# Kernel tuning notes

Hardware: AMD Instinct MI355X
Metric: run time of the kernel (lower is better)

Reference implementation:

```python
import jax, jax.numpy as jnp
import numpy as np

D = 1024      # input_dim / hidden_size
H = 16        # n_heads
HD = D // H   # head_size = 64
F = 4096      # mlp_dim
EPS = 1e-6


def setup_inputs() -> dict:
    key = jax.random.key(0)
    ks = jax.random.split(key, 16)
    s = 0.02
    inp = {
        "x": jax.random.normal(ks[0], (4, 2048, D), dtype=jnp.float32),
        # attention params (torch Linear: y = x @ W.T + b; we store W as [out,in])
        "Wq": jax.random.normal(ks[1], (D, D), dtype=jnp.float32) * s,
        "bq": jax.random.normal(ks[2], (D,), dtype=jnp.float32) * s,
        "Wk": jax.random.normal(ks[3], (D, D), dtype=jnp.float32) * s,
        "bk": jax.random.normal(ks[4], (D,), dtype=jnp.float32) * s,
        "Wv": jax.random.normal(ks[5], (D, D), dtype=jnp.float32) * s,
        "bv": jax.random.normal(ks[6], (D,), dtype=jnp.float32) * s,
        "Wo": jax.random.normal(ks[7], (D, D), dtype=jnp.float32) * s,
        "bo": jax.random.normal(ks[8], (D,), dtype=jnp.float32) * s,
        # MLP params
        "W1": jax.random.normal(ks[9], (F, D), dtype=jnp.float32) * s,
        "b1": jax.random.normal(ks[10], (F,), dtype=jnp.float32) * s,
        "W2": jax.random.normal(ks[11], (D, F), dtype=jnp.float32) * s,
        "b2": jax.random.normal(ks[12], (D,), dtype=jnp.float32) * s,
        # LayerNorm params
        "ln1_g": jnp.ones((D,), dtype=jnp.float32),
        "ln1_b": jnp.zeros((D,), dtype=jnp.float32),
        "ln2_g": jnp.ones((D,), dtype=jnp.float32),
        "ln2_b": jnp.zeros((D,), dtype=jnp.float32),
    }
    return inp


def _layernorm(x, g, b):
    mu = jnp.mean(x, axis=-1, keepdims=True)
    var = jnp.mean(jnp.square(x - mu), axis=-1, keepdims=True)
    return (x - mu) * jax.lax.rsqrt(var + EPS) * g + b


def reference(x, Wq, bq, Wk, bk, Wv, bv, Wo, bo, W1, b1, W2, b2,
              ln1_g, ln1_b, ln2_g, ln2_b):
    B, S, _ = x.shape
    h = x
    xn = _layernorm(x, ln1_g, ln1_b)
    # Q/K/V projections -> [B, H, S, HD]
    def split_heads(t):
        return t.reshape(B, S, H, HD).transpose(0, 2, 1, 3)
    q = split_heads(xn @ Wq.T + bq)
    k = split_heads(xn @ Wk.T + bk)
    v = split_heads(xn @ Wv.T + bv)
    scores = jnp.einsum('bhqd,bhkd->bhqk', q, k) / np.sqrt(HD).astype(np.float32)
    probs = jax.nn.softmax(scores, axis=-1)
    ctx = jnp.einsum('bhqk,bhkd->bhqd', probs, v)      # [B,H,S,HD]
    ctx = ctx.transpose(0, 2, 1, 3).reshape(B, S, D)
    attn_out = ctx @ Wo.T + bo
    x = attn_out + h
    h = x
    xn = _layernorm(x, ln2_g, ln2_b)
    y = jax.nn.gelu(xn @ W1.T + b1, approximate=False)  # torch nn.GELU() = exact erf gelu
    y = y @ W2.T + b2
    return y + h
```

## Files before the change

kernel.cpp:

```cpp
#include <hip/hip_runtime.h>
#include <hip/hip_bf16.h>
#include <math.h>

typedef __attribute__((ext_vector_type(8))) short short8;
typedef __attribute__((ext_vector_type(4))) float f32x4;

#define MFMA_BF16 __builtin_amdgcn_mfma_f32_16x16x32_bf16

__device__ __forceinline__ ushort f2bf(float f) {
  union { __hip_bfloat16 h; ushort u; } c;
  c.h = __float2bfloat16(f);
  return c.u;
}
__device__ __forceinline__ void async_cp16(const ushort* g, ushort* l) {
  __builtin_amdgcn_global_load_lds(
      (const __attribute__((address_space(1))) void*)g,
      (__attribute__((address_space(3))) void*)l, 16, 0, 0);
}

__global__ __launch_bounds__(256) void conv_all(
    const float* __restrict__ Wq, const float* __restrict__ Wk,
    const float* __restrict__ Wv, const float* __restrict__ Wo,
    const float* __restrict__ W1, const float* __restrict__ W2,
    const float* __restrict__ bq, const float* __restrict__ bk,
    const float* __restrict__ bv,
    ushort* __restrict__ wqkv, ushort* __restrict__ wo,
    ushort* __restrict__ w1, ushort* __restrict__ w2,
    float* __restrict__ bqkv) {
  int i = blockIdx.x * 256 + threadIdx.x;
  if (i < 3145728) {
    const float* src; ushort* dst; int off;
    if (i < 786432)        {
      dst = wqkv; off = i;
      if (i < 262144)      src = Wq + (size_t)i * 4;
      else if (i < 524288) src = Wk + (size_t)(i - 262144) * 4;
      else                 src = Wv + (size_t)(i - 524288) * 4;
    } else if (i < 1048576) { dst = wo; off = i - 786432;  src = Wo + (size_t)off * 4; }
    else if (i < 2097152)   { dst = w1; off = i - 1048576; src = W1 + (size_t)off * 4; }
    else                    { dst = w2; off = i - 2097152; src = W2 + (size_t)off * 4; }
    float4 v = *(const float4*)src;
    ushort4 o;
    o.x = f2bf(v.x); o.y = f2bf(v.y); o.z = f2bf(v.z); o.w = f2bf(v.w);
    ((ushort4*)dst)[off] = o;
  } else if (i < 3146496) {
    int off = i - 3145728;
    const float* src;
    if (off < 256)      src = bq + (size_t)off * 4;
    else if (off < 512) src = bk + (size_t)(off - 256) * 4;
    else                src = bv + (size_t)(off - 512) * 4;
    ((float4*)bqkv)[off] = *(const float4*)src;
  }
}

__global__ __launch_bounds__(256) void ln_kernel(const float* __restrict__ x,
    const float* __restrict__ g, const float* __restrict__ b,
    ushort* __restrict__ out) {
  const int row = blockIdx.x, t = threadIdx.x;
  float4 v = ((const float4*)(x + (size_t)row * 1024))[t];
  float s  = v.x + v.y + v.z + v.w;
  float ss = v.x*v.x + v.y*v.y + v.z*v.z + v.w*v.w;
  #pragma unroll
  for (int off = 32; off >= 1; off >>= 1) {
    s  += __shfl_xor(s, off);
    ss += __shfl_xor(ss, off);
  }
  __shared__ float red[8];
  int wv = t >> 6, ln = t & 63;
  if (ln == 0) { red[wv] = s; red[4 + wv] = ss; }
  __syncthreads();
  float S  = red[0] + red[1] + red[2] + red[3];
  float SS = red[4] + red[5] + red[6] + red[7];
  float mu  = S * (1.0f/1024.0f);
  float var = SS * (1.0f/1024.0f) - mu*mu;
  float rs  = rsqrtf(var + 1e-6f);
  float4 gv = ((const float4*)g)[t];
  float4 bv = ((const float4*)b)[t];
  ushort4 o;
  o.x = f2bf((v.x-mu)*rs*gv.x + bv.x);
  o.y = f2bf((v.y-mu)*rs*gv.y + bv.y);
  o.z = f2bf((v.z-mu)*rs*gv.z + bv.z);
  o.w = f2bf((v.w-mu)*rs*gv.w + bv.w);
  ((ushort4*)(out + (size_t)row*1024))[t] = o;
}

enum { EPI_QK = 0, EPI_VT = 1, EPI_WO = 2, EPI_GELU = 3, EPI_OUT = 4 };

template <int EPI>
__global__ __launch_bounds__(512, 2) void gemm256_kernel(const ushort* __restrict__ A,
    const ushort* __restrict__ Bw, const float* __restrict__ bias,
    void* __restrict__ outp, void* __restrict__ outp2, int K, int N, float scale) {
  __shared__ ushort As[2][256 * 64];
  __shared__ ushort Bs[2][256 * 64];
  const int t = threadIdx.x;
  const int lane = t & 63, wave = t >> 6;
  const int col = lane & 15, quad = lane >> 4;
  const int m0 = blockIdx.x * 256, n0 = blockIdx.y * 256;
  const int wm = wave >> 2, wn = wave & 3;

  f32x4 acc[8][4];
  #pragma unroll
  for (int i = 0; i < 8; i++)
    #pragma unroll
    for (int j = 0; j < 4; j++)
      acc[i][j] = (f32x4){0.f, 0.f, 0.f, 0.f};

  size_t aoff[2], boff[2];
  int d0[2];
  #pragma unroll
  for (int i = 0; i < 2; i++) {
    int c = i * 512 + t, r = c >> 3, p = c & 7;
    aoff[i] = (size_t)(m0 + r) * K + (p ^ (r & 7)) * 8;
    boff[i] = (size_t)(n0 + r) * K + (p ^ (r & 7)) * 8;
    d0[i] = c * 8;
  }
  const size_t up = (size_t)128 * K;

  const int NT = K >> 6;
  #pragma unroll
  for (int i = 0; i < 2; i++) async_cp16(A  + aoff[i],      &As[0][d0[i]]);
  #pragma unroll
  for (int i = 0; i < 2; i++) async_cp16(Bw + boff[i],      &Bs[0][d0[i]]);
  #pragma unroll
  for (int i = 0; i < 2; i++) async_cp16(A  + aoff[i] + up, &As[0][8192 + d0[i]]);
  #pragma unroll
  for (int i = 0; i < 2; i++) async_cp16(Bw + boff[i] + up, &Bs[0][8192 + d0[i]]);
  asm volatile("s_waitcnt vmcnt(4)" ::: "memory");
  __builtin_amdgcn_sched_barrier(0);
  __builtin_amdgcn_s_barrier();
  __builtin_amdgcn_sched_barrier(0);

  short8 af0[4][2], af1[4][2], bf[2][2];
  for (int kt = 0; kt < NT; kt++) {
    const int cur = kt & 1, nxt = cur ^ 1;
    const size_t ko = (size_t)(kt + 1) << 6;
    const bool more = (kt + 1 < NT);

    #pragma unroll
    for (int tml = 0; tml < 4; tml++) {
      const int row = wm * 64 + tml * 16 + col;
      #pragma unroll
      for (int c = 0; c < 2; c++)
        af0[tml][c] = *(const short8*)&As[cur][row * 64 + (((c * 4 + quad) ^ (row & 7)) * 8)];
    }
    #pragma unroll
    for (int tnl = 0; tnl < 2; tnl++) {
      const int row = wn * 32 + tnl * 16 + col;
      #pragma unroll
      for (int c = 0; c < 2; c++)
        bf[tnl][c] = *(const short8*)&Bs[cur][row * 64 + (((c * 4 + quad) ^ (row & 7)) * 8)];
    }
    if (more) {
      #pragma unroll
      for (int i = 0; i < 2; i++) async_cp16(A + aoff[i] + ko, &As[nxt][d0[i]]);
      asm volatile("s_waitcnt vmcnt(4)" ::: "memory");
    } else {
      asm volatile("s_waitcnt vmcnt(2)" ::: "memory");
    }
    __builtin_amdgcn_sched_barrier(0);
    __builtin_amdgcn_s_barrier();
    asm volatile("s_waitcnt lgkmcnt(0)" ::: "memory");
    __builtin_amdgcn_sched_barrier(0);
    __builtin_amdgcn_s_setprio(1);
    #pragma unroll
    for (int tml = 0; tml < 4; tml++)
      #pragma unroll
      for (int tnl = 0; tnl < 2; tnl++) {
        acc[tml][tnl] = MFMA_BF16(af0[tml][0], bf[tnl][0], acc[tml][tnl], 0, 0, 0);
        acc[tml][tnl] = MFMA_BF16(af0[tml][1], bf[tnl][1], acc[tml][tnl], 0, 0, 0);
      }
    __builtin_amdgcn_s_setprio(0);
    __builtin_amdgcn_sched_barrier(0);
    __builtin_amdgcn_s_barrier();
    __builtin_amdgcn_sched_barrier(0);

    #pragma unroll
    for (int tml = 0; tml < 4; tml++) {
      const int row = 128 + wm * 64 + tml * 16 + col;
      #pragma unroll
      for (int c = 0; c < 2; c++)
        af1[tml][c] = *(const short8*)&As[cur][row * 64 + (((c * 4 + quad) ^ (row & 7)) * 8)];
    }
    if (more) {
      #pragma unroll
      for (int i = 0; i < 2; i++) async_cp16(Bw + boff[i] + ko, &Bs[nxt][d0[i]]);
      asm volatile("s_waitcnt vmcnt(4)" ::: "memory");
    } else {
      asm volatile("s_waitcnt vmcnt(0)" ::: "memory");
    }
    __builtin_amdgcn_sched_barrier(0);
    __builtin_amdgcn_s_barrier();
    asm volatile("s_waitcnt lgkmcnt(0)" ::: "memory");
    __builtin_amdgcn_sched_barrier(0);
    __builtin_amdgcn_s_setprio(1);
    #pragma unroll
    for (int tml = 0; tml < 4; tml++)
      #pragma unroll
      for (int tnl = 0; tnl < 2; tnl++) {
        acc[4+tml][tnl] = MFMA_BF16(af1[tml][0], bf[tnl][0], acc[4+tml][tnl], 0, 0, 0);
        acc[4+tml][tnl] = MFMA_BF16(af1[tml][1], bf[tnl][1], acc[4+tml][tnl], 0, 0, 0);
      }
    __builtin_amdgcn_s_setprio(0);
    __builtin_amdgcn_sched_barrier(0);
    __builtin_amdgcn_s_barrier();
    __builtin_amdgcn_sched_barrier(0);

    #pragma unroll
    for (int tnl = 0; tnl < 2; tnl++) {
      const int row = 128 + wn * 32 + tnl * 16 + col;
      #pragma unroll
      for (int c = 0; c < 2; c++)
        bf[tnl][c] = *(const short8*)&Bs[cur][row * 64 + (((c * 4 + quad) ^ (row & 7)) * 8)];
    }
    if (more) {
      #pragma unroll
      for (int i = 0; i < 2; i++) async_cp16(A + aoff[i] + up + ko, &As[nxt][8192 + d0[i]]);
      asm volatile("s_waitcnt vmcnt(4)" ::: "memory");
    } else {
      asm volatile("s_waitcnt vmcnt(0)" ::: "memory");
    }
    __builtin_amdgcn_sched_barrier(0);
    __builtin_amdgcn_s_barrier();
    asm volatile("s_waitcnt lgkmcnt(0)" ::: "memory");
    __builtin_amdgcn_sched_barrier(0);
    __builtin_amdgcn_s_setprio(1);
    #pragma unroll
    for (int tml = 0; tml < 4; tml++)
      #pragma unroll
      for (int tnl = 0; tnl < 2; tnl++) {
        acc[tml][2+tnl] = MFMA_BF16(af0[tml][0], bf[tnl][0], acc[tml][2+tnl], 0, 0, 0);
        acc[tml][2+tnl] = MFMA_BF16(af0[tml][1], bf[tnl][1], acc[tml][2+tnl], 0, 0, 0);
      }
    __builtin_amdgcn_s_setprio(0);
    __builtin_amdgcn_sched_barrier(0);
    __builtin_amdgcn_s_barrier();
    __builtin_amdgcn_sched_barrier(0);

    if (more) {
      #pragma unroll
      for (int i = 0; i < 2; i++) async_cp16(Bw + boff[i] + up + ko, &Bs[nxt][8192 + d0[i]]);
      asm volatile("s_waitcnt vmcnt(4)" ::: "memory");
    } else {
      asm volatile("s_waitcnt vmcnt(0)" ::: "memory");
    }
    __builtin_amdgcn_sched_barrier(0);
    __builtin_amdgcn_s_barrier();
    asm volatile("s_waitcnt lgkmcnt(0)" ::: "memory");
    __builtin_amdgcn_sched_barrier(0);
    __builtin_amdgcn_s_setprio(1);
    #pragma unroll
    for (int tml = 0; tml < 4; tml++)
      #pragma unroll
      for (int tnl = 0; tnl < 2; tnl++) {
        acc[4+tml][2+tnl] = MFMA_BF16(af1[tml][0], bf[tnl][0], acc[4+tml][2+tnl], 0, 0, 0);
        acc[4+tml][2+tnl] = MFMA_BF16(af1[tml][1], bf[tnl][1], acc[4+tml][2+tnl], 0, 0, 0);
      }
    __builtin_amdgcn_s_setprio(0);
    __builtin_amdgcn_sched_barrier(0);
    __builtin_amdgcn_s_barrier();
    __builtin_amdgcn_sched_barrier(0);
  }

  #pragma unroll
  for (int tm = 0; tm < 8; tm++) {
    const int ha = tm >> 2, tml = tm & 3;
    #pragma unroll
    for (int tn = 0; tn < 4; tn++) {
      const int hb = tn >> 1, tnl = tn & 1;
      const int n = n0 + hb * 128 + wn * 32 + tnl * 16 + col;
      const float bn = bias[n];
      #pragma unroll
      for (int r = 0; r < 4; r++) {
        const int m = m0 + ha * 128 + wm * 64 + tml * 16 + quad * 4 + r;
        float v = acc[tm][tn][r] + bn;
        if (EPI == EPI_QK) {
          int nl = n & 1023, h = nl >> 6, hd = nl & 63;
          int bb = m >> 11, s2 = m & 2047;
          if (n < 1024)
            ((ushort*)outp)[(((size_t)(bb * 16 + h) * 2048 + s2) * 64) + hd] = f2bf(v * scale);
          else
            ((ushort*)outp2)[(((size_t)(bb * 16 + h) * 2048 + s2) * 64) + hd] = f2bf(v);
        } else {
          float u = v * 0.7978845608028654f * (1.0f + 0.044715f * v * v);
          float e = __builtin_amdgcn_exp2f(u * 2.885390081777927f);
          float th = 1.0f - 2.0f * __builtin_amdgcn_rcpf(e + 1.0f);
          ((ushort*)outp)[(size_t)m * N + n] = f2bf(0.5f * v * (1.0f + th));
        }
      }
    }
  }
}

template <int EPI>
__global__ __launch_bounds__(512, 2) void gemmW_kernel(const ushort* __restrict__ A,
    const ushort* __restrict__ Bw, const float* __restrict__ bias,
    const float* __restrict__ res, void* __restrict__ outp, int K, int N) {
  __shared__ ushort As[2][256 * 64];
  __shared__ ushort Bs[2][128 * 64];
  const int t = threadIdx.x;
  const int lane = t & 63, wave = t >> 6;
  const int col = lane & 15, quad = lane >> 4;
  const int m0 = blockIdx.x * 256, n0 = blockIdx.y * 128;
  const int wm = wave >> 1, wn = wave & 1;

  f32x4 acc[4][4];
  #pragma unroll
  for (int i = 0; i < 4; i++)
    #pragma unroll
    for (int j = 0; j < 4; j++)
      acc[i][j] = (f32x4){0.f, 0.f, 0.f, 0.f};

  size_t aoff[2];
  int ad0[2];
  #pragma unroll
  for (int i = 0; i < 2; i++) {
    int c = i * 512 + t, r = c >> 3, p = c & 7;
    aoff[i] = (size_t)(m0 + r) * K + (p ^ (r & 7)) * 8;
    ad0[i] = c * 8;
  }
  size_t boff;
  int bd0;
  {
    int c = t, r = c >> 3, p = c & 7;
    boff = (size_t)(n0 + r) * K + (p ^ (r & 7)) * 8;
    bd0 = c * 8;
  }
  const size_t upA = (size_t)128 * K;
  const size_t upB = (size_t)64 * K;

  const int NT = K >> 6;
  #pragma unroll
  for (int i = 0; i < 2; i++) async_cp16(A + aoff[i], &As[0][ad0[i]]);
  async_cp16(Bw + boff, &Bs[0][bd0]);
  #pragma unroll
  for (int i = 0; i < 2; i++) async_cp16(A + aoff[i] + upA, &As[0][8192 + ad0[i]]);
  async_cp16(Bw + boff + upB, &Bs[0][4096 + bd0]);
  asm volatile("s_waitcnt vmcnt(3)" ::: "memory");
  __builtin_amdgcn_sched_barrier(0);
  __builtin_amdgcn_s_barrier();
  __builtin_amdgcn_sched_barrier(0);

  short8 af0[2][2], af1[2][2], bf[2][2];
  for (int kt = 0; kt < NT; kt++) {
    const int cur = kt & 1, nxt = cur ^ 1;
    const size_t ko = (size_t)(kt + 1) << 6;
    const bool more = (kt + 1 < NT);

    #pragma unroll
    for (int tml = 0; tml < 2; tml++) {
      const int row = wm * 32 + tml * 16 + col;
      #pragma unroll
      for (int c = 0; c < 2; c++)
        af0[tml][c] = *(const short8*)&As[cur][row * 64 + (((c * 4 + quad) ^ (row & 7)) * 8)];
    }
    #pragma unroll
    for (int tnl = 0; tnl < 2; tnl++) {
      const int row = wn * 32 + tnl * 16 + col;
      #pragma unroll
      for (int c = 0; c < 2; c++)
        bf[tnl][c] = *(const short8*)&Bs[cur][row * 64 + (((c * 4 + quad) ^ (row & 7)) * 8)];
    }
    if (more) {
      #pragma unroll
      for (int i = 0; i < 2; i++) async_cp16(A + aoff[i] + ko, &As[nxt][ad0[i]]);
      asm volatile("s_waitcnt vmcnt(3)" ::: "memory");
    } else {
      asm volatile("s_waitcnt vmcnt(1)" ::: "memory");
    }
    __builtin_amdgcn_sched_barrier(0);
    __builtin_amdgcn_s_barrier();
    asm volatile("s_waitcnt lgkmcnt(0)" ::: "memory");
    __builtin_amdgcn_sched_barrier(0);
    __builtin_amdgcn_s_setprio(1);
    #pragma unroll
    for (int tml = 0; tml < 2; tml++)
      #pragma unroll
      for (int tnl = 0; tnl < 2; tnl++) {
        acc[tml][tnl] = MFMA_BF16(af0[tml][0], bf[tnl][0], acc[tml][tnl], 0, 0, 0);
        acc[tml][tnl] = MFMA_BF16(af0[tml][1], bf[tnl][1], acc[tml][tnl], 0, 0, 0);
      }
    __builtin_amdgcn_s_setprio(0);
    __builtin_amdgcn_sched_barrier(0);
    __builtin_amdgcn_s_barrier();
    __builtin_amdgcn_sched_barrier(0);

    #pragma unroll
    for (int tml = 0; tml < 2; tml++) {
      const int row = 128 + wm * 32 + tml * 16 + col;
      #pragma unroll
      for (int c = 0; c < 2; c++)
        af1[tml][c] = *(const short8*)&As[cur][row * 64 + (((c * 4 + quad) ^ (row & 7)) * 8)];
    }
    if (more) {
      async_cp16(Bw + boff + ko, &Bs[nxt][bd0]);
      asm volatile("s_waitcnt vmcnt(3)" ::: "memory");
    } else {
      asm volatile("s_waitcnt vmcnt(0)" ::: "memory");
    }
    __builtin_amdgcn_sched_barrier(0);
    __builtin_amdgcn_s_barrier();
    asm volatile("s_waitcnt lgkmcnt(0)" ::: "memory");
    __builtin_amdgcn_sched_barrier(0);
    __builtin_amdgcn_s_setprio(1);
    #pragma unroll
    for (int tml = 0; tml < 2; tml++)
      #pragma unroll
      for (int tnl = 0; tnl < 2; tnl++) {
        acc[2+tml][tnl] = MFMA_BF16(af1[tml][0], bf[tnl][0], acc[2+tml][tnl], 0, 0, 0);
        acc[2+tml][tnl] = MFMA_BF16(af1[tml][1], bf[tnl][1], acc[2+tml][tnl], 0, 0, 0);
      }
    __builtin_amdgcn_s_setprio(0);
    __builtin_amdgcn_sched_barrier(0);
    __builtin_amdgcn_s_barrier();
    __builtin_amdgcn_sched_barrier(0);

    #pragma unroll
    for (int tnl = 0; tnl < 2; tnl++) {
      const int row = 64 + wn * 32 + tnl * 16 + col;
      #pragma unroll
      for (int c = 0; c < 2; c++)
        bf[tnl][c] = *(const short8*)&Bs[cur][4096 + ((row - 64) * 64) + (((c * 4 + quad) ^ (row & 7)) * 8)];
    }
    if (more) {
      #pragma unroll
      for (int i = 0; i < 2; i++) async_cp16(A + aoff[i] + upA + ko, &As[nxt][8192 + ad0[i]]);
      asm volatile("s_waitcnt vmcnt(5)" ::: "memory");
    } else {
      asm volatile("s_waitcnt vmcnt(0)" ::: "memory");
    }
    __builtin_amdgcn_sched_barrier(0);
    __builtin_amdgcn_s_barrier();
    asm volatile("s_waitcnt lgkmcnt(0)" ::: "memory");
    __builtin_amdgcn_sched_barrier(0);
    __builtin_amdgcn_s_setprio(1);
    #pragma unroll
    for (int tml = 0; tml < 2; tml++)
      #pragma unroll
      for (int tnl = 0; tnl < 2; tnl++) {
        acc[tml][2+tnl] = MFMA_BF16(af0[tml][0], bf[tnl][0], acc[tml][2+tnl], 0, 0, 0);
        acc[tml][2+tnl] = MFMA_BF16(af0[tml][1], bf[tnl][1], acc[tml][2+tnl], 0, 0, 0);
      }
    __builtin_amdgcn_s_setprio(0);
    __builtin_amdgcn_sched_barrier(0);
    __builtin_amdgcn_s_barrier();
    __builtin_amdgcn_sched_barrier(0);

    if (more) {
      async_cp16(Bw + boff + upB + ko, &Bs[nxt][4096 + bd0]);
      asm volatile("s_waitcnt vmcnt(3)" ::: "memory");
    } else {
      asm volatile("s_waitcnt vmcnt(0)" ::: "memory");
    }
    __builtin_amdgcn_sched_barrier(0);
    __builtin_amdgcn_s_barrier();
    asm volatile("s_waitcnt lgkmcnt(0)" ::: "memory");
    __builtin_amdgcn_sched_barrier(0);
    __builtin_amdgcn_s_setprio(1);
    #pragma unroll
    for (int tml = 0; tml < 2; tml++)
      #pragma unroll
      for (int tnl = 0; tnl < 2; tnl++) {
        acc[2+tml][2+tnl] = MFMA_BF16(af1[tml][0], bf[tnl][0], acc[2+tml][2+tnl], 0, 0, 0);
        acc[2+tml][2+tnl] = MFMA_BF16(af1[tml][1], bf[tnl][1], acc[2+tml][2+tnl], 0, 0, 0);
      }
    __builtin_amdgcn_s_setprio(0);
    __builtin_amdgcn_sched_barrier(0);
    __builtin_amdgcn_s_barrier();
    __builtin_amdgcn_sched_barrier(0);
  }

  #pragma unroll
  for (int tm = 0; tm < 4; tm++) {
    const int ha = tm >> 1, tml = tm & 1;
    #pragma unroll
    for (int tn = 0; tn < 4; tn++) {
      const int hb = tn >> 1, tnl = tn & 1;
      const int n = n0 + hb * 64 + wn * 32 + tnl * 16 + col;
      #pragma unroll
      for (int r = 0; r < 4; r++) {
        const int m = m0 + ha * 128 + wm * 32 + tml * 16 + quad * 4 + r;
        float v = acc[tm][tn][r];
        if (EPI == EPI_VT) {
          float vv = v + bias[m];
          int h = m >> 6, hd = m & 63, bb = n >> 11, s2 = n & 2047;
          ((ushort*)outp)[((size_t)((bb * 16 + h) * 64 + hd)) * 2048 + s2] = f2bf(vv);
        } else {
          ((float*)outp)[(size_t)m * N + n] = v + bias[n] + res[(size_t)m * N + n];
        }
      }
    }
  }
}

__global__ __launch_bounds__(256) void attn_kernel(const ushort* __restrict__ Qb,
    const ushort* __restrict__ Kb, const ushort* __restrict__ Vt,
    ushort* __restrict__ ctx) {
  const int lane = threadIdx.x & 63, wave = threadIdx.x >> 6;
  const int col = lane & 15, quad = lane >> 4;
  const int bx = blockIdx.x;
  const int bh = bx & 63;
  const int qt = bx >> 6;
  const int qbase = qt * 128 + wave * 32;
  const ushort* Qh = Qb + (size_t)bh * 2048 * 64;
  const ushort* Kh = Kb + (size_t)bh * 2048 * 64;
  const ushort* Vh = Vt + (size_t)bh * 64 * 2048;

  short8 qa[2][2];
  #pragma unroll
  for (int qg = 0; qg < 2; qg++) {
    const ushort* Qr = Qh + (size_t)(qbase + qg * 16 + col) * 64 + quad * 8;
    qa[qg][0] = *(const short8*)Qr;
    qa[qg][1] = *(const short8*)(Qr + 32);
  }

  short8 ones8;
  #pragma unroll
  for (int i = 0; i < 8; i++) ones8[i] = (short)0x3F80;

  f32x4 Ot[2][4], Ol[2];
  #pragma unroll
  for (int qg = 0; qg < 2; qg++) {
    Ol[qg] = (f32x4){0.f, 0.f, 0.f, 0.f};
    #pragma unroll
    for (int dt = 0; dt < 4; dt++) Ot[qg][dt] = (f32x4){0.f, 0.f, 0.f, 0.f};
  }

  __shared__ ushort Ks[2][2][64 * 32];
  __shared__ ushort Vs[2][2][64 * 32];
  __shared__ ushort P_lds[4][16][64];

  const int lrow = lane >> 2;
  const int srow = wave * 16 + lrow;
  const int lcol = ((lane & 3) ^ ((srow >> 1) & 3)) * 8;
  const ushort* Kg = Kh + (size_t)srow * 64 + lcol;
  const ushort* Vg = Vh + (size_t)srow * 2048 + lcol;
  const int so = (wave * 16) * 32;

  const int kvswz = (col >> 1) & 3;
  const int pswz = col & 7;

  async_cp16(Kg,      &Ks[0][0][so]);
  async_cp16(Kg + 32, &Ks[0][1][so]);
  async_cp16(Vg,      &Vs[0][0][so]);
  async_cp16(Vg + 32, &Vs[0][1][so]);
  __syncthreads();

  int cur = 0;
  for (int kb = 0; kb < 2048; kb += 64) {
    if (kb + 64 < 2048) {
      const int nxt = cur ^ 1;
      async_cp16(Kg + (size_t)(kb + 64) * 64,      &Ks[nxt][0][so]);
      async_cp16(Kg + (size_t)(kb + 64) * 64 + 32, &Ks[nxt][1][so]);
      async_cp16(Vg + (kb + 64),                   &Vs[nxt][0][so]);
      async_cp16(Vg + (kb + 64) + 32,              &Vs[nxt][1][so]);
    }

    short8 kf[4][2], vf[4][2];
    #pragma unroll
    for (int kt = 0; kt < 4; kt++)
      #pragma unroll
      for (int c = 0; c < 2; c++)
        kf[kt][c] = *(const short8*)&Ks[cur][c][(kt * 16 + col) * 32 + (quad ^ kvswz) * 8];
    #pragma unroll
    for (int dt = 0; dt < 4; dt++)
      #pragma unroll
      for (int c = 0; c < 2; c++)
        vf[dt][c] = *(const short8*)&Vs[cur][c][(dt * 16 + col) * 32 + (quad ^ kvswz) * 8];

    #pragma unroll
    for (int qg = 0; qg < 2; qg++) {
      f32x4 s[4];
      __builtin_amdgcn_s_setprio(1);
      #pragma unroll
      for (int kt = 0; kt < 4; kt++) {
        s[kt] = (f32x4){0.f, 0.f, 0.f, 0.f};
        s[kt] = MFMA_BF16(kf[kt][0], qa[qg][0], s[kt], 0, 0, 0);
        s[kt] = MFMA_BF16(kf[kt][1], qa[qg][1], s[kt], 0, 0, 0);
      }
      __builtin_amdgcn_s_setprio(0);
      ushort(*P)[64] = P_lds[wave];
      #pragma unroll
      for (int kt = 0; kt < 4; kt++) {
        float p0 = __builtin_amdgcn_exp2f(s[kt][0]);
        float p1 = __builtin_amdgcn_exp2f(s[kt][1]);
        float p2 = __builtin_amdgcn_exp2f(s[kt][2]);
        float p3 = __builtin_amdgcn_exp2f(s[kt][3]);
        uint2 pk;
        asm("v_cvt_pk_bf16_f32 %0, %1, %2" : "=v"(pk.x) : "v"(p0), "v"(p1));
        asm("v_cvt_pk_bf16_f32 %0, %1, %2" : "=v"(pk.y) : "v"(p2), "v"(p3));
        *(uint2*)&P[col][(((2 * kt + (quad >> 1)) ^ pswz) * 8) + (quad & 1) * 4] = pk;
      }
      #pragma unroll
      for (int c = 0; c < 2; c++) {
        short8 pf = *(const short8*)&P_lds[wave][col][((4 * c + quad) ^ pswz) * 8];
        __builtin_amdgcn_s_setprio(1);
        #pragma unroll
        for (int dt = 0; dt < 4; dt++)
          Ot[qg][dt] = MFMA_BF16(vf[dt][c], pf, Ot[qg][dt], 0, 0, 0);
        Ol[qg] = MFMA_BF16(ones8, pf, Ol[qg], 0, 0, 0);
        __builtin_amdgcn_s_setprio(0);
      }
    }
    __syncthreads();
    cur ^= 1;
  }

  const int bb = bh >> 4, h = bh & 15;
  #pragma unroll
  for (int qg = 0; qg < 2; qg++) {
    float inv = __builtin_amdgcn_rcpf(Ol[qg][0]);
    const int q = qbase + qg * 16 + col;
    size_t base = ((size_t)(bb * 2048 + q)) * 1024 + h * 64;
    #pragma unroll
    for (int dt = 0; dt < 4; dt++) {
      ushort4 o;
      o.x = f2bf(Ot[qg][dt][0] * inv);
      o.y = f2bf(Ot[qg][dt][1] * inv);
      o.z = f2bf(Ot[qg][dt][2] * inv);
      o.w = f2bf(Ot[qg][dt][3] * inv);
      *(ushort4*)&ctx[base + dt * 16 + quad * 4] = o;
    }
  }
}

extern "C" void kernel_launch(void* const* d_in, const int* in_sizes, int n_in,
                              void* d_out, int out_size, void* d_ws, size_t ws_size,
                              hipStream_t stream) {
  const float* x     = (const float*)d_in[0];
  const float* Wq    = (const float*)d_in[1];
  const float* bq    = (const float*)d_in[2];
  const float* Wk    = (const float*)d_in[3];
  const float* bk    = (const float*)d_in[4];
  const float* Wv    = (const float*)d_in[5];
  const float* bv    = (const float*)d_in[6];
  const float* Wo    = (const float*)d_in[7];
  const float* bo    = (const float*)d_in[8];
  const float* W1    = (const float*)d_in[9];
  const float* b1    = (const float*)d_in[10];
  const float* W2    = (const float*)d_in[11];
  const float* b2    = (const float*)d_in[12];
  const float* ln1_g = (const float*)d_in[13];
  const float* ln1_b = (const float*)d_in[14];
  const float* ln2_g = (const float*)d_in[15];
  const float* ln2_b = (const float*)d_in[16];

  const size_t MB = 1ull << 20;
  char* ws = (char*)d_ws;
  ushort* Wqkv_b = (ushort*)(ws + 0 * MB);
  ushort* Wo_b   = (ushort*)(ws + 6 * MB);
  ushort* W1_b   = (ushort*)(ws + 8 * MB);
  ushort* W2_b   = (ushort*)(ws + 16 * MB);
  ushort* xn1    = (ushort*)(ws + 24 * MB);
  ushort* Qb     = (ushort*)(ws + 40 * MB);
  ushort* Kb     = (ushort*)(ws + 56 * MB);
  ushort* Vt     = (ushort*)(ws + 72 * MB);
  ushort* ctxb   = (ushort*)(ws + 88 * MB);
  float*  x2     = (float*)(ws + 104 * MB);
  ushort* xn2    = (ushort*)(ws + 136 * MB);
  ushort* y1     = (ushort*)(ws + 152 * MB);
  float*  bqkv   = (float*)(ws + 152 * MB);

  conv_all<<<12291, 256, 0, stream>>>(Wq, Wk, Wv, Wo, W1, W2, bq, bk, bv,
                                      Wqkv_b, Wo_b, W1_b, W2_b, bqkv);

  ln_kernel<<<8192, 256, 0, stream>>>(x, ln1_g, ln1_b, xn1);

  const float cs = 0.125f * 1.4426950408889634f;
  gemm256_kernel<EPI_QK><<<dim3(32, 8), 512, 0, stream>>>(
      xn1, Wqkv_b, bqkv, Qb, Kb, 1024, 2048, cs);
  gemmW_kernel<EPI_VT><<<dim3(4, 64), 512, 0, stream>>>(
      Wqkv_b + (size_t)2048 * 1024, xn1, bqkv + 2048, nullptr, Vt, 1024, 8192);

  attn_kernel<<<1024, 256, 0, stream>>>(Qb, Kb, Vt, ctxb);

  gemmW_kernel<EPI_WO><<<dim3(32, 8), 512, 0, stream>>>(
      ctxb, Wo_b, bo, x, x2, 1024, 1024);

  ln_kernel<<<8192, 256, 0, stream>>>(x2, ln2_g, ln2_b, xn2);

  gemm256_kernel<EPI_GELU><<<dim3(32, 16), 512, 0, stream>>>(
      xn2, W1_b, b1, y1, nullptr, 1024, 4096, 1.0f);
  gemmW_kernel<EPI_OUT><<<dim3(32, 8), 512, 0, stream>>>(
      y1, W2_b, b2, x2, d_out, 4096, 1024);
}
```

Measured before the change: 518.6 us.

## Transpose GEMM tile to 128x256 with 2x4 waves and XCD-aware block remap

Replaces the 256x128 gemmW kernel with a gemmH kernel that uses a 128(M)x256(N) tile, a 2x4 wave layout where each wave holds 64x64, and two MFMA phases per k-step instead of four. It also swizzles the 1D block index so that consecutive blocks on the same XCD share tiles, aiming at better L2 reuse. The goal is fewer barriers per k-step and more register reuse of A fragments, at the cost of a changed load/wait schedule and a remapped grid that must divide evenly for each launch.

```diff
diff --git a/kernel.cpp b/kernel.cpp
--- a/kernel.cpp
+++ b/kernel.cpp
@@ -291,16 +291,17 @@
 }
 
 template <int EPI>
-__global__ __launch_bounds__(512, 2) void gemmW_kernel(const ushort* __restrict__ A,
+__global__ __launch_bounds__(512, 2) void gemmH_kernel(const ushort* __restrict__ A,
     const ushort* __restrict__ Bw, const float* __restrict__ bias,
-    const float* __restrict__ res, void* __restrict__ outp, int K, int N) {
-  __shared__ ushort As[2][256 * 64];
-  __shared__ ushort Bs[2][128 * 64];
+    const float* __restrict__ res, void* __restrict__ outp, int K, int N, int gx) {
+  __shared__ ushort As[2][128 * 64];
+  __shared__ ushort Bs[2][256 * 64];
   const int t = threadIdx.x;
   const int lane = t & 63, wave = t >> 6;
   const int col = lane & 15, quad = lane >> 4;
-  const int m0 = blockIdx.x * 256, n0 = blockIdx.y * 128;
-  const int wm = wave >> 1, wn = wave & 1;
+  const int bl = (blockIdx.x & 7) * 32 + (blockIdx.x >> 3);
+  const int m0 = (bl % gx) * 128, n0 = (bl / gx) * 256;
+  const int wm = wave >> 2, wn = wave & 3;
 
   f32x4 acc[4][4];
   #pragma unroll
@@ -309,48 +310,41 @@
     for (int j = 0; j < 4; j++)
       acc[i][j] = (f32x4){0.f, 0.f, 0.f, 0.f};
 
-  size_t aoff[2];
-  int ad0[2];
+  size_t aoff[2], boff[2];
+  int ad0[2], bd0[2];
   #pragma unroll
   for (int i = 0; i < 2; i++) {
     int c = i * 512 + t, r = c >> 3, p = c & 7;
     aoff[i] = (size_t)(m0 + r) * K + (p ^ (r & 7)) * 8;
-    ad0[i] = c * 8;
-  }
-  size_t boff;
-  int bd0;
-  {
-    int c = t, r = c >> 3, p = c & 7;
-    boff = (size_t)(n0 + r) * K + (p ^ (r & 7)) * 8;
-    bd0 = c * 8;
-  }
-  const size_t upA = (size_t)128 * K;
-  const size_t upB = (size_t)64 * K;
+    boff[i] = (size_t)(n0 + r) * K + (p ^ (r & 7)) * 8;
+    ad0[i] = c * 8; bd0[i] = c * 8;
+  }
+  const size_t upB = (size_t)128 * K;
 
   const int NT = K >> 6;
   #pragma unroll
-  for (int i = 0; i < 2; i++) async_cp16(A + aoff[i], &As[0][ad0[i]]);
-  async_cp16(Bw + boff, &Bs[0][bd0]);
-  #pragma unroll
-  for (int i = 0; i < 2; i++) async_cp16(A + aoff[i] + upA, &As[0][8192 + ad0[i]]);
-  async_cp16(Bw + boff + upB, &Bs[0][4096 + bd0]);
-  asm volatile("s_waitcnt vmcnt(3)" ::: "memory");
+  for (int i = 0; i < 2; i++) async_cp16(A  + aoff[i],       &As[0][ad0[i]]);
+  #pragma unroll
+  for (int i = 0; i < 2; i++) async_cp16(Bw + boff[i],       &Bs[0][bd0[i]]);
+  #pragma unroll
+  for (int i = 0; i < 2; i++) async_cp16(Bw + boff[i] + upB, &Bs[0][8192 + bd0[i]]);
+  asm volatile("s_waitcnt vmcnt(2)" ::: "memory");
   __builtin_amdgcn_sched_barrier(0);
   __builtin_amdgcn_s_barrier();
   __builtin_amdgcn_sched_barrier(0);
 
-  short8 af0[2][2], af1[2][2], bf[2][2];
+  short8 af[4][2], bf[2][2];
   for (int kt = 0; kt < NT; kt++) {
     const int cur = kt & 1, nxt = cur ^ 1;
     const size_t ko = (size_t)(kt + 1) << 6;
     const bool more = (kt + 1 < NT);
 
     #pragma unroll
-    for (int tml = 0; tml < 2; tml++) {
-      const int row = wm * 32 + tml * 16 + col;
-      #pragma unroll
-      for (int c = 0; c < 2; c++)
-        af0[tml][c] = *(const short8*)&As[cur][row * 64 + (((c * 4 + quad) ^ (row & 7)) * 8)];
+    for (int tml = 0; tml < 4; tml++) {
+      const int row = wm * 64 + tml * 16 + col;
+      #pragma unroll
+      for (int c = 0; c < 2; c++)
+        af[tml][c] = *(const short8*)&As[cur][row * 64 + (((c * 4 + quad) ^ (row & 7)) * 8)];
     }
     #pragma unroll
     for (int tnl = 0; tnl < 2; tnl++) {
@@ -361,38 +355,10 @@
     }
     if (more) {
       #pragma unroll
-      for (int i = 0; i < 2; i++) async_cp16(A + aoff[i] + ko, &As[nxt][ad0[i]]);
-      asm volatile("s_waitcnt vmcnt(3)" ::: "memory");
-    } else {
-      asm volatile("s_waitcnt vmcnt(1)" ::: "memory");
-    }
-    __builtin_amdgcn_sched_barrier(0);
-    __builtin_amdgcn_s_barrier();
-    asm volatile("s_waitcnt lgkmcnt(0)" ::: "memory");
-    __builtin_amdgcn_sched_barrier(0);
-    __builtin_amdgcn_s_setprio(1);
-    #pragma unroll
-    for (int tml = 0; tml < 2; tml++)
-      #pragma unroll
-      for (int tnl = 0; tnl < 2; tnl++) {
-        acc[tml][tnl] = MFMA_BF16(af0[tml][0], bf[tnl][0], acc[tml][tnl], 0, 0, 0);
-        acc[tml][tnl] = MFMA_BF16(af0[tml][1], bf[tnl][1], acc[tml][tnl], 0, 0, 0);
-      }
-    __builtin_amdgcn_s_setprio(0);
-    __builtin_amdgcn_sched_barrier(0);
-    __builtin_amdgcn_s_barrier();
-    __builtin_amdgcn_sched_barrier(0);
-
-    #pragma unroll
-    for (int tml = 0; tml < 2; tml++) {
-      const int row = 128 + wm * 32 + tml * 16 + col;
-      #pragma unroll
-      for (int c = 0; c < 2; c++)
-        af1[tml][c] = *(const short8*)&As[cur][row * 64 + (((c * 4 + quad) ^ (row & 7)) * 8)];
-    }
-    if (more) {
-      async_cp16(Bw + boff + ko, &Bs[nxt][bd0]);
-      asm volatile("s_waitcnt vmcnt(3)" ::: "memory");
+      for (int i = 0; i < 2; i++) async_cp16(A  + aoff[i] + ko, &As[nxt][ad0[i]]);
+      #pragma unroll
+      for (int i = 0; i < 2; i++) async_cp16(Bw + boff[i] + ko, &Bs[nxt][bd0[i]]);
+      asm volatile("s_waitcnt vmcnt(4)" ::: "memory");
     } else {
       asm volatile("s_waitcnt vmcnt(0)" ::: "memory");
     }
@@ -402,11 +368,11 @@
     __builtin_amdgcn_sched_barrier(0);
     __builtin_amdgcn_s_setprio(1);
     #pragma unroll
-    for (int tml = 0; tml < 2; tml++)
+    for (int tml = 0; tml < 4; tml++)
       #pragma unroll
       for (int tnl = 0; tnl < 2; tnl++) {
-        acc[2+tml][tnl] = MFMA_BF16(af1[tml][0], bf[tnl][0], acc[2+tml][tnl], 0, 0, 0);
-        acc[2+tml][tnl] = MFMA_BF16(af1[tml][1], bf[tnl][1], acc[2+tml][tnl], 0, 0, 0);
+        acc[tml][tnl] = MFMA_BF16(af[tml][0], bf[tnl][0], acc[tml][tnl], 0, 0, 0);
+        acc[tml][tnl] = MFMA_BF16(af[tml][1], bf[tnl][1], acc[tml][tnl], 0, 0, 0);
       }
     __builtin_amdgcn_s_setprio(0);
     __builtin_amdgcn_sched_barrier(0);
@@ -415,15 +381,15 @@
 
     #pragma unroll
     for (int tnl = 0; tnl < 2; tnl++) {
-      const int row = 64 + wn * 32 + tnl * 16 + col;
-      #pragma unroll
-      for (int c = 0; c < 2; c++)
-        bf[tnl][c] = *(const short8*)&Bs[cur][4096 + ((row - 64) * 64) + (((c * 4 + quad) ^ (row & 7)) * 8)];
+      const int rp = wn * 32 + tnl * 16 + col;
+      #pragma unroll
+      for (int c = 0; c < 2; c++)
+        bf[tnl][c] = *(const short8*)&Bs[cur][8192 + rp * 64 + (((c * 4 + quad) ^ (rp & 7)) * 8)];
     }
     if (more) {
       #pragma unroll
-      for (int i = 0; i < 2; i++) async_cp16(A + aoff[i] + upA + ko, &As[nxt][8192 + ad0[i]]);
-      asm volatile("s_waitcnt vmcnt(5)" ::: "memory");
+      for (int i = 0; i < 2; i++) async_cp16(Bw + boff[i] + upB + ko, &Bs[nxt][8192 + bd0[i]]);
+      asm volatile("s_waitcnt vmcnt(2)" ::: "memory");
     } else {
       asm volatile("s_waitcnt vmcnt(0)" ::: "memory");
     }
@@ -433,52 +399,28 @@
     __builtin_amdgcn_sched_barrier(0);
     __builtin_amdgcn_s_setprio(1);
     #pragma unroll
-    for (int tml = 0; tml < 2; tml++)
+    for (int tml = 0; tml < 4; tml++)
       #pragma unroll
       for (int tnl = 0; tnl < 2; tnl++) {
-        acc[tml][2+tnl] = MFMA_BF16(af0[tml][0], bf[tnl][0], acc[tml][2+tnl], 0, 0, 0);
-        acc[tml][2+tnl] = MFMA_BF16(af0[tml][1], bf[tnl][1], acc[tml][2+tnl], 0, 0, 0);
+        acc[tml][2+tnl] = MFMA_BF16(af[tml][0], bf[tnl][0], acc[tml][2+tnl], 0, 0, 0);
+        acc[tml][2+tnl] = MFMA_BF16(af[tml][1], bf[tnl][1], acc[tml][2+tnl], 0, 0, 0);
       }
     __builtin_amdgcn_s_setprio(0);
     __builtin_amdgcn_sched_barrier(0);
     __builtin_amdgcn_s_barrier();
     __builtin_amdgcn_sched_barrier(0);
-
-    if (more) {
-      async_cp16(Bw + boff + upB + ko, &Bs[nxt][4096 + bd0]);
-      asm volatile("s_waitcnt vmcnt(3)" ::: "memory");
-    } else {
-      asm volatile("s_waitcnt vmcnt(0)" ::: "memory");
-    }
-    __builtin_amdgcn_sched_barrier(0);
-    __builtin_amdgcn_s_barrier();
-    asm volatile("s_waitcnt lgkmcnt(0)" ::: "memory");
-    __builtin_amdgcn_sched_barrier(0);
-    __builtin_amdgcn_s_setprio(1);
-    #pragma unroll
-    for (int tml = 0; tml < 2; tml++)
-      #pragma unroll
-      for (int tnl = 0; tnl < 2; tnl++) {
-        acc[2+tml][2+tnl] = MFMA_BF16(af1[tml][0], bf[tnl][0], acc[2+tml][2+tnl], 0, 0, 0);
-        acc[2+tml][2+tnl] = MFMA_BF16(af1[tml][1], bf[tnl][1], acc[2+tml][2+tnl], 0, 0, 0);
-      }
-    __builtin_amdgcn_s_setprio(0);
-    __builtin_amdgcn_sched_barrier(0);
-    __builtin_amdgcn_s_barrier();
-    __builtin_amdgcn_sched_barrier(0);
-  }
-
-  #pragma unroll
-  for (int tm = 0; tm < 4; tm++) {
-    const int ha = tm >> 1, tml = tm & 1;
+  }
+
+  #pragma unroll
+  for (int tml = 0; tml < 4; tml++) {
     #pragma unroll
     for (int tn = 0; tn < 4; tn++) {
       const int hb = tn >> 1, tnl = tn & 1;
-      const int n = n0 + hb * 64 + wn * 32 + tnl * 16 + col;
+      const int n = n0 + hb * 128 + wn * 32 + tnl * 16 + col;
       #pragma unroll
       for (int r = 0; r < 4; r++) {
-        const int m = m0 + ha * 128 + wm * 32 + tml * 16 + quad * 4 + r;
-        float v = acc[tm][tn][r];
+        const int m = m0 + wm * 64 + tml * 16 + quad * 4 + r;
+        float v = acc[tml][tn][r];
         if (EPI == EPI_VT) {
           float vv = v + bias[m];
           int h = m >> 6, hd = m & 63, bb = n >> 11, s2 = n & 2047;
@@ -667,18 +609,18 @@
   const float cs = 0.125f * 1.4426950408889634f;
   gemm256_kernel<EPI_QK><<<dim3(32, 8), 512, 0, stream>>>(
       xn1, Wqkv_b, bqkv, Qb, Kb, 1024, 2048, cs);
-  gemmW_kernel<EPI_VT><<<dim3(4, 64), 512, 0, stream>>>(
-      Wqkv_b + (size_t)2048 * 1024, xn1, bqkv + 2048, nullptr, Vt, 1024, 8192);
+  gemmH_kernel<EPI_VT><<<256, 512, 0, stream>>>(
+      Wqkv_b + (size_t)2048 * 1024, xn1, bqkv + 2048, nullptr, Vt, 1024, 8192, 8);
 
   attn_kernel<<<1024, 256, 0, stream>>>(Qb, Kb, Vt, ctxb);
 
-  gemmW_kernel<EPI_WO><<<dim3(32, 8), 512, 0, stream>>>(
-      ctxb, Wo_b, bo, x, x2, 1024, 1024);
+  gemmH_kernel<EPI_WO><<<256, 512, 0, stream>>>(
+      ctxb, Wo_b, bo, x, x2, 1024, 1024, 64);
 
   ln_kernel<<<8192, 256, 0, stream>>>(x2, ln2_g, ln2_b, xn2);
 
   gemm256_kernel<EPI_GELU><<<dim3(32, 16), 512, 0, stream>>>(
       xn2, W1_b, b1, y1, nullptr, 1024, 4096, 1.0f);
-  gemmW_kernel<EPI_OUT><<<dim3(32, 8), 512, 0, stream>>>(
-      y1, W2_b, b2, x2, d_out, 4096, 1024);
-}
+  gemmH_kernel<EPI_OUT><<<256, 512, 0, stream>>>(
+      y1, W2_b, b2, x2, d_out, 4096, 1024, 64);
+}
```

After: 499.9 us. 1.04x faster.
